# Optimization experiments

Hardware: AMD Instinct MI355X
Metric: run time of the kernel (lower is better)

The kernel has to match this reference:

```python
import jax, jax.numpy as jnp
import numpy as np

B, H, L, E, MODES = 32, 8, 4096, 64, 64


def setup_inputs() -> dict:
    key = jax.random.key(0)
    kx, kw, ki = jax.random.split(key, 3)
    x = jax.random.normal(kx, (B, H, L, E), dtype=jnp.float32)
    # nn.Parameter(torch.randn(E, E, modes, 2) / sqrt(E))
    weights = jax.random.normal(kw, (E, E, MODES, 2), dtype=jnp.float32) / np.sqrt(E)
    # register_buffer: sorted random permutation of [0, seq_len//2) truncated to modes (unique)
    index = jnp.sort(jax.random.permutation(ki, L // 2)[:MODES]).astype(jnp.int64)
    return {"x": x, "weights": weights, "index": index}


def reference(x, weights, index):
    # x: [B, H, L, E]
    Bs, Hs, Ls, Es = x.shape
    xt = jnp.swapaxes(x, -1, -2)                 # [B, H, E, L]
    x_ft = jnp.fft.rfft(xt, axis=-1)             # [B, H, E, L//2+1] complex64
    w_c = weights[..., 0] + 1j * weights[..., 1]  # [E, E, modes] complex
    sel = x_ft[..., index]                       # gather selected modes: [B, H, E, modes]
    out_sel = jnp.einsum('bhei,eoi->bhoi', sel, w_c)  # [B, H, E_out, modes]
    out_ft = jnp.zeros_like(x_ft).at[..., index].set(out_sel)  # scatter into zero spectrum
    y = jnp.fft.irfft(out_ft, n=Ls, axis=-1)     # [B, H, E, L]
    return jnp.swapaxes(y, -1, -2)               # [B, H, L, E]
```

## Files before the change

### kernel.cpp

```cpp
#include <hip/hip_runtime.h>
#include <hip/hip_bf16.h>
#include <math.h>

#define LTOT   4096
#define EDIM   64
#define NMODES 64
#define BH     256
#define TWO_PI 6.28318530717958647692f

typedef float f32x4 __attribute__((ext_vector_type(4)));
typedef short s16x8 __attribute__((ext_vector_type(8)));

__device__ inline unsigned short f2bf(float f) {
    unsigned u = __builtin_bit_cast(unsigned, f);
    u += 0x7fff + ((u >> 16) & 1);
    return (unsigned short)(u >> 16);
}
__device__ inline unsigned packbf(float lo, float hi) {
    float2 t; t.x = lo; t.y = hi;
    __hip_bfloat162 h = __float22bfloat162_rn(t);
    unsigned r;
    __builtin_memcpy(&r, &h, 4);
    return r;
}
__device__ inline float bf2f(unsigned lo16) {
    return __builtin_bit_cast(float, lo16 << 16);
}

__global__ void k_tab_m(const int* __restrict__ index, unsigned short* __restrict__ Tm) {
    int k = blockIdx.x;
    int f = index[k];
    for (int l = threadIdx.x; l < LTOT; l += blockDim.x) {
        int m = (f * l) & (LTOT - 1);
        float th = (float)m * (TWO_PI / (float)LTOT);
        float s, c; sincosf(th, &s, &c);
        Tm[(size_t)(2 * k) * LTOT + l]     = f2bf(c);
        Tm[(size_t)(2 * k + 1) * LTOT + l] = f2bf(-s);
    }
}
__global__ void k_tab_t(const int* __restrict__ index, unsigned short* __restrict__ Tt) {
    int l = blockIdx.x * 4 + (threadIdx.x >> 6);
    int k = threadIdx.x & 63;
    int f = index[k];
    int m = (f * l) & (LTOT - 1);
    float th = (float)m * (TWO_PI / (float)LTOT);
    float s, c; sincosf(th, &s, &c);
    ((unsigned*)Tt)[l * 64 + k] = packbf(c, s);
}
__global__ void k_wtab(const float* __restrict__ w, unsigned* __restrict__ wt) {
    int i = blockIdx.x * 256 + threadIdx.x;
    float2 v = ((const float2*)w)[i];
    wt[i] = packbf(v.x, v.y);
}

__global__ __launch_bounds__(256, 4) void k_stage1(const float* __restrict__ x,
                                                   const unsigned short* __restrict__ Tm,
                                                   float* __restrict__ Xp) {
    int bh = blockIdx.x >> 2, part = blockIdx.x & 3;
    const float* xb = x + ((size_t)bh * LTOT + part * 1024) * EDIM;
    __shared__ unsigned xT[2][64 * 68];

    int t = threadIdx.x;
    int q = t & 15, lp0 = t >> 4;
    int lane = t & 63, w = t >> 6;
    int r = lane & 15, kb8 = lane >> 4;
    int es = w & 1, ms = w >> 1;
    unsigned swzW = ((unsigned)(q & 7)) << 2;

    f32x4 acc[2][4];
    #pragma unroll
    for (int i = 0; i < 2; ++i)
        #pragma unroll
        for (int n = 0; n < 4; ++n) acc[i][n] = (f32x4)0.f;

    float4 xn[8];
    #pragma unroll
    for (int p = 0; p < 4; ++p) {
        const float* b = xb + (size_t)(2 * (lp0 + p * 16)) * EDIM + 4 * q;
        xn[2 * p]     = *(const float4*)b;
        xn[2 * p + 1] = *(const float4*)(b + EDIM);
    }
    #pragma unroll
    for (int p = 0; p < 4; ++p) {
        float A0[4] = {xn[2*p].x, xn[2*p].y, xn[2*p].z, xn[2*p].w};
        float A1[4] = {xn[2*p+1].x, xn[2*p+1].y, xn[2*p+1].z, xn[2*p+1].w};
        #pragma unroll
        for (int j = 0; j < 4; ++j)
            xT[0][(4 * q + j) * 68 + (((unsigned)(lp0 + p * 16)) ^ swzW)] = packbf(A0[j], A1[j]);
    }
    __syncthreads();

    for (int t8 = 0; t8 < 8; ++t8) {
        int cur = t8 & 1;
        if (t8 < 7) {
            const float* tb = xb + (size_t)((t8 + 1) * 128) * EDIM;
            #pragma unroll
            for (int p = 0; p < 4; ++p) {
                const float* b = tb + (size_t)(2 * (lp0 + p * 16)) * EDIM + 4 * q;
                xn[2 * p]     = *(const float4*)b;
                xn[2 * p + 1] = *(const float4*)(b + EDIM);
            }
        }
        #pragma unroll
        for (int kk = 0; kk < 4; ++kk) {
            s16x8 af[2];
            #pragma unroll
            for (int sub = 0; sub < 2; ++sub) {
                int row = es * 32 + sub * 16 + r;
                unsigned swz = (((unsigned)sub) << 4) + (((unsigned)(r >> 2)) << 2);
                af[sub] = *(const s16x8*)(xT[cur] + row * 68 + (((unsigned)(kk * 16 + kb8 * 4)) ^ swz));
            }
            #pragma unroll
            for (int ns = 0; ns < 4; ++ns) {
                int m = ms * 64 + ns * 16 + r;
                s16x8 bf = *(const s16x8*)(Tm + (size_t)m * LTOT + part * 1024 + t8 * 128 + kk * 32 + kb8 * 8);
                acc[0][ns] = __builtin_amdgcn_mfma_f32_16x16x32_bf16(af[0], bf, acc[0][ns], 0, 0, 0);
                acc[1][ns] = __builtin_amdgcn_mfma_f32_16x16x32_bf16(af[1], bf, acc[1][ns], 0, 0, 0);
            }
        }
        if (t8 < 7) {
            #pragma unroll
            for (int p = 0; p < 4; ++p) {
                float A0[4] = {xn[2*p].x, xn[2*p].y, xn[2*p].z, xn[2*p].w};
                float A1[4] = {xn[2*p+1].x, xn[2*p+1].y, xn[2*p+1].z, xn[2*p+1].w};
                #pragma unroll
                for (int j = 0; j < 4; ++j)
                    xT[cur ^ 1][(4 * q + j) * 68 + (((unsigned)(lp0 + p * 16)) ^ swzW)] = packbf(A0[j], A1[j]);
            }
        }
        __syncthreads();
    }

    float* Xb = Xp + ((size_t)part * BH + bh) * (64 * 128);
    #pragma unroll
    for (int sub = 0; sub < 2; ++sub)
        #pragma unroll
        for (int ns = 0; ns < 4; ++ns)
            #pragma unroll
            for (int g = 0; g < 4; ++g)
                Xb[(es * 32 + sub * 16 + kb8 * 4 + g) * 128 + ms * 64 + ns * 16 + r] = acc[sub][ns][g];
}

__global__ __launch_bounds__(512, 4) void k_stage23(const float* __restrict__ Xp,
                                                    const unsigned* __restrict__ wtab,
                                                    const unsigned short* __restrict__ Tt,
                                                    const int* __restrict__ index,
                                                    float* __restrict__ y) {
    int bh = blockIdx.x;
    __shared__ float XsR[64 * 68];
    __shared__ float XsI[64 * 68];
    __shared__ unsigned ABl[64 * 68];

    int t = threadIdx.x;
    int lane = t & 63, w = t >> 6;
    int r = lane & 15, kb8 = lane >> 4;

    #pragma unroll
    for (int i = 0; i < 4; ++i) {
        int idx = t + i * 512;
        f32x4 v = (f32x4)0.f;
        #pragma unroll
        for (int p = 0; p < 4; ++p)
            v += ((const f32x4*)(Xp + ((size_t)p * BH + bh) * 8192))[idx];
        int e = idx >> 5, k0 = (idx & 31) * 2;
        XsR[e * 68 + k0]     = v.x;
        XsI[e * 68 + k0]     = v.y;
        XsR[e * 68 + k0 + 1] = v.z;
        XsI[e * 68 + k0 + 1] = v.w;
    }
    __syncthreads();

    {
        int k = lane;
        int f = index[k];
        float cc = (f == 0 ? 1.0f : 2.0f) / (float)LTOT;
        int o0 = w * 8;
        float aR[8] = {}, aI[8] = {};
        for (int e = 0; e < 64; ++e) {
            float xr = XsR[e * 68 + k];
            float xi = XsI[e * 68 + k];
            #pragma unroll
            for (int oi = 0; oi < 8; ++oi) {
                unsigned wv = wtab[((size_t)(e * 64 + o0 + oi)) * 64 + k];
                float wr = bf2f(wv & 0xffffu);
                float wi = bf2f(wv >> 16);
                aR[oi] += xr * wr - xi * wi;
                aI[oi] += xr * wi + xi * wr;
            }
        }
        #pragma unroll
        for (int oi = 0; oi < 8; ++oi) {
            float im = (f == 0) ? 0.0f : -cc * aI[oi];
            ABl[(o0 + oi) * 68 + k] = packbf(cc * aR[oi], im);
        }
    }
    __syncthreads();

    s16x8 afr[4][4];
    #pragma unroll
    for (int es2 = 0; es2 < 4; ++es2)
        #pragma unroll
        for (int ks = 0; ks < 4; ++ks)
            afr[es2][ks] = *(const s16x8*)((const unsigned short*)ABl +
                                           (es2 * 16 + r) * 136 + ks * 32 + kb8 * 8);

    for (int it = 0; it < 32; ++it) {
        int ltile = w * 512 + it * 16;
        s16x8 btf[4];
        #pragma unroll
        for (int ks = 0; ks < 4; ++ks)
            btf[ks] = *(const s16x8*)(Tt + (size_t)(ltile + r) * 128 + ks * 32 + kb8 * 8);
        f32x4 oa[4];
        #pragma unroll
        for (int es2 = 0; es2 < 4; ++es2) oa[es2] = (f32x4)0.f;
        #pragma unroll
        for (int ks = 0; ks < 4; ++ks)
            #pragma unroll
            for (int es2 = 0; es2 < 4; ++es2)
                oa[es2] = __builtin_amdgcn_mfma_f32_16x16x32_bf16(afr[es2][ks], btf[ks], oa[es2], 0, 0, 0);
        float* yb = y + ((size_t)bh * LTOT + ltile + r) * EDIM;
        #pragma unroll
        for (int es2 = 0; es2 < 4; ++es2)
            *(f32x4*)(yb + es2 * 16 + kb8 * 4) = oa[es2];
    }
}

extern "C" void kernel_launch(void* const* d_in, const int* in_sizes, int n_in,
                              void* d_out, int out_size, void* d_ws, size_t ws_size,
                              hipStream_t stream) {
    const float* x     = (const float*)d_in[0];
    const float* wgt   = (const float*)d_in[1];
    const int*   index = (const int*)d_in[2];
    float* y  = (float*)d_out;
    float* ws = (float*)d_ws;

    unsigned short* Tm = (unsigned short*)ws;
    unsigned short* Tt = (unsigned short*)(ws + 262144);
    unsigned*       wt = (unsigned*)(ws + 524288);
    float*          Xp = ws + 786432;

    hipLaunchKernelGGL(k_tab_m,   dim3(NMODES), dim3(256), 0, stream, index, Tm);
    hipLaunchKernelGGL(k_tab_t,   dim3(1024),   dim3(256), 0, stream, index, Tt);
    hipLaunchKernelGGL(k_wtab,    dim3(1024),   dim3(256), 0, stream, wgt, wt);
    hipLaunchKernelGGL(k_stage1,  dim3(BH * 4), dim3(256), 0, stream, x, Tm, Xp);
    hipLaunchKernelGGL(k_stage23, dim3(BH),     dim3(512), 0, stream, Xp, wt, Tt, index, y);
}
```

Measured before the change: 220.7 us.

## Merge table kernels, single-buffer stage1 LDS, split stage23 into more-parallel stage2/stage3

The three table-building kernels become one launch. Stage1 drops its double-buffered LDS tile for a single buffer with an extra barrier, and raises the occupancy hint to 5 blocks. The fused stage23 kernel, which ran only 256 blocks, is split into a mixing kernel that writes bf16 coefficients to global memory and a synthesis kernel with 4x as many blocks, to use more CUs for the output-bound inverse transform. The cost is an extra launch, a global round trip for the coefficients, and less overlap of loads with compute in stage1.

```diff
diff --git a/kernel.cpp b/kernel.cpp
--- a/kernel.cpp
+++ b/kernel.cpp
@@ -27,38 +27,41 @@
     return __builtin_bit_cast(float, lo16 << 16);
 }
 
-__global__ void k_tab_m(const int* __restrict__ index, unsigned short* __restrict__ Tm) {
-    int k = blockIdx.x;
-    int f = index[k];
-    for (int l = threadIdx.x; l < LTOT; l += blockDim.x) {
+__global__ __launch_bounds__(256) void k_tables(const int* __restrict__ index,
+                                                const float* __restrict__ w,
+                                                unsigned short* __restrict__ Tm,
+                                                unsigned short* __restrict__ Tt,
+                                                unsigned* __restrict__ wt) {
+    int b = blockIdx.x, t = threadIdx.x;
+    if (b < 64) {
+        int k = b, f = index[k];
+        for (int l = t; l < LTOT; l += 256) {
+            int m = (f * l) & (LTOT - 1);
+            float th = (float)m * (TWO_PI / (float)LTOT);
+            float s, c; sincosf(th, &s, &c);
+            Tm[(size_t)(2 * k) * LTOT + l]     = f2bf(c);
+            Tm[(size_t)(2 * k + 1) * LTOT + l] = f2bf(-s);
+        }
+    } else if (b < 64 + 1024) {
+        int l = (b - 64) * 4 + (t >> 6);
+        int k = t & 63, f = index[k];
         int m = (f * l) & (LTOT - 1);
         float th = (float)m * (TWO_PI / (float)LTOT);
         float s, c; sincosf(th, &s, &c);
-        Tm[(size_t)(2 * k) * LTOT + l]     = f2bf(c);
-        Tm[(size_t)(2 * k + 1) * LTOT + l] = f2bf(-s);
-    }
-}
-__global__ void k_tab_t(const int* __restrict__ index, unsigned short* __restrict__ Tt) {
-    int l = blockIdx.x * 4 + (threadIdx.x >> 6);
-    int k = threadIdx.x & 63;
-    int f = index[k];
-    int m = (f * l) & (LTOT - 1);
-    float th = (float)m * (TWO_PI / (float)LTOT);
-    float s, c; sincosf(th, &s, &c);
-    ((unsigned*)Tt)[l * 64 + k] = packbf(c, s);
-}
-__global__ void k_wtab(const float* __restrict__ w, unsigned* __restrict__ wt) {
-    int i = blockIdx.x * 256 + threadIdx.x;
-    float2 v = ((const float2*)w)[i];
-    wt[i] = packbf(v.x, v.y);
-}
-
-__global__ __launch_bounds__(256, 4) void k_stage1(const float* __restrict__ x,
+        ((unsigned*)Tt)[l * 64 + k] = packbf(c, s);
+    } else {
+        int i = (b - 1088) * 256 + t;
+        float2 v = ((const float2*)w)[i];
+        wt[i] = packbf(v.x, v.y);
+    }
+}
+
+__global__ __launch_bounds__(256, 5) void k_stage1(const float* __restrict__ x,
                                                    const unsigned short* __restrict__ Tm,
                                                    float* __restrict__ Xp) {
     int bh = blockIdx.x >> 2, part = blockIdx.x & 3;
     const float* xb = x + ((size_t)bh * LTOT + part * 1024) * EDIM;
-    __shared__ unsigned xT[2][64 * 68];
+    __shared__ unsigned xT[64 * 68];
 
     int t = threadIdx.x;
     int q = t & 15, lp0 = t >> 4;
@@ -74,31 +77,31 @@
         for (int n = 0; n < 4; ++n) acc[i][n] = (f32x4)0.f;
 
     float4 xn[8];
-    #pragma unroll
-    for (int p = 0; p < 4; ++p) {
-        const float* b = xb + (size_t)(2 * (lp0 + p * 16)) * EDIM + 4 * q;
-        xn[2 * p]     = *(const float4*)b;
-        xn[2 * p + 1] = *(const float4*)(b + EDIM);
-    }
-    #pragma unroll
-    for (int p = 0; p < 4; ++p) {
-        float A0[4] = {xn[2*p].x, xn[2*p].y, xn[2*p].z, xn[2*p].w};
-        float A1[4] = {xn[2*p+1].x, xn[2*p+1].y, xn[2*p+1].z, xn[2*p+1].w};
-        #pragma unroll
-        for (int j = 0; j < 4; ++j)
-            xT[0][(4 * q + j) * 68 + (((unsigned)(lp0 + p * 16)) ^ swzW)] = packbf(A0[j], A1[j]);
-    }
-    __syncthreads();
-
+    {
+        #pragma unroll
+        for (int p = 0; p < 4; ++p) {
+            const float* bp = xb + (size_t)(2 * (lp0 + p * 16)) * EDIM + 4 * q;
+            xn[2 * p]     = *(const float4*)bp;
+            xn[2 * p + 1] = *(const float4*)(bp + EDIM);
+        }
+    }
     for (int t8 = 0; t8 < 8; ++t8) {
-        int cur = t8 & 1;
+        #pragma unroll
+        for (int p = 0; p < 4; ++p) {
+            float A0[4] = {xn[2*p].x, xn[2*p].y, xn[2*p].z, xn[2*p].w};
+            float A1[4] = {xn[2*p+1].x, xn[2*p+1].y, xn[2*p+1].z, xn[2*p+1].w};
+            #pragma unroll
+            for (int j = 0; j < 4; ++j)
+                xT[(4 * q + j) * 68 + (((unsigned)(lp0 + p * 16)) ^ swzW)] = packbf(A0[j], A1[j]);
+        }
+        __syncthreads();
         if (t8 < 7) {
             const float* tb = xb + (size_t)((t8 + 1) * 128) * EDIM;
             #pragma unroll
             for (int p = 0; p < 4; ++p) {
-                const float* b = tb + (size_t)(2 * (lp0 + p * 16)) * EDIM + 4 * q;
-                xn[2 * p]     = *(const float4*)b;
-                xn[2 * p + 1] = *(const float4*)(b + EDIM);
+                const float* bp = tb + (size_t)(2 * (lp0 + p * 16)) * EDIM + 4 * q;
+                xn[2 * p]     = *(const float4*)bp;
+                xn[2 * p + 1] = *(const float4*)(bp + EDIM);
             }
         }
         #pragma unroll
@@ -108,7 +111,7 @@
             for (int sub = 0; sub < 2; ++sub) {
                 int row = es * 32 + sub * 16 + r;
                 unsigned swz = (((unsigned)sub) << 4) + (((unsigned)(r >> 2)) << 2);
-                af[sub] = *(const s16x8*)(xT[cur] + row * 68 + (((unsigned)(kk * 16 + kb8 * 4)) ^ swz));
+                af[sub] = *(const s16x8*)(xT + row * 68 + (((unsigned)(kk * 16 + kb8 * 4)) ^ swz));
             }
             #pragma unroll
             for (int ns = 0; ns < 4; ++ns) {
@@ -118,16 +121,6 @@
                 acc[1][ns] = __builtin_amdgcn_mfma_f32_16x16x32_bf16(af[1], bf, acc[1][ns], 0, 0, 0);
             }
         }
-        if (t8 < 7) {
-            #pragma unroll
-            for (int p = 0; p < 4; ++p) {
-                float A0[4] = {xn[2*p].x, xn[2*p].y, xn[2*p].z, xn[2*p].w};
-                float A1[4] = {xn[2*p+1].x, xn[2*p+1].y, xn[2*p+1].z, xn[2*p+1].w};
-                #pragma unroll
-                for (int j = 0; j < 4; ++j)
-                    xT[cur ^ 1][(4 * q + j) * 68 + (((unsigned)(lp0 + p * 16)) ^ swzW)] = packbf(A0[j], A1[j]);
-            }
-        }
         __syncthreads();
     }
 
@@ -141,19 +134,14 @@
                 Xb[(es * 32 + sub * 16 + kb8 * 4 + g) * 128 + ms * 64 + ns * 16 + r] = acc[sub][ns][g];
 }
 
-__global__ __launch_bounds__(512, 4) void k_stage23(const float* __restrict__ Xp,
-                                                    const unsigned* __restrict__ wtab,
-                                                    const unsigned short* __restrict__ Tt,
-                                                    const int* __restrict__ index,
-                                                    float* __restrict__ y) {
+__global__ __launch_bounds__(512) void k_stage2(const float* __restrict__ Xp,
+                                                const unsigned* __restrict__ wtab,
+                                                const int* __restrict__ index,
+                                                unsigned* __restrict__ ABo) {
     int bh = blockIdx.x;
     __shared__ float XsR[64 * 68];
     __shared__ float XsI[64 * 68];
-    __shared__ unsigned ABl[64 * 68];
-
     int t = threadIdx.x;
-    int lane = t & 63, w = t >> 6;
-    int r = lane & 15, kb8 = lane >> 4;
 
     #pragma unroll
     for (int i = 0; i < 4; ++i) {
@@ -170,58 +158,77 @@
     }
     __syncthreads();
 
+    int k = t & 63, og = t >> 6;
+    int f = index[k];
+    float cc = (f == 0 ? 1.0f : 2.0f) / (float)LTOT;
+    int o0 = og * 8;
+    float aR[8] = {}, aI[8] = {};
+    for (int e = 0; e < 64; ++e) {
+        float xr = XsR[e * 68 + k];
+        float xi = XsI[e * 68 + k];
+        #pragma unroll
+        for (int oi = 0; oi < 8; ++oi) {
+            unsigned wv = wtab[((size_t)(e * 64 + o0 + oi)) * 64 + k];
+            float wr = bf2f(wv & 0xffffu);
+            float wi = bf2f(wv >> 16);
+            aR[oi] += xr * wr - xi * wi;
+            aI[oi] += xr * wi + xi * wr;
+        }
+    }
+    #pragma unroll
+    for (int oi = 0; oi < 8; ++oi) {
+        float im = (f == 0) ? 0.0f : -cc * aI[oi];
+        ABo[((size_t)bh * 64 + o0 + oi) * 64 + k] = packbf(cc * aR[oi], im);
+    }
+}
+
+#define S3P16 136
+__global__ __launch_bounds__(256, 4) void k_stage3(const unsigned short* __restrict__ Tt,
+                                                   const unsigned* __restrict__ ABo,
+                                                   float* __restrict__ y) {
+    int bh = blockIdx.x >> 2, qtr = blockIdx.x & 3;
+    __shared__ unsigned short ABl[64 * S3P16];
+    int t = threadIdx.x;
+    int lane = t & 63, wave = t >> 6;
+    int r = lane & 15, kb8 = lane >> 4;
+
     {
-        int k = lane;
-        int f = index[k];
-        float cc = (f == 0 ? 1.0f : 2.0f) / (float)LTOT;
-        int o0 = w * 8;
-        float aR[8] = {}, aI[8] = {};
-        for (int e = 0; e < 64; ++e) {
-            float xr = XsR[e * 68 + k];
-            float xi = XsI[e * 68 + k];
-            #pragma unroll
-            for (int oi = 0; oi < 8; ++oi) {
-                unsigned wv = wtab[((size_t)(e * 64 + o0 + oi)) * 64 + k];
-                float wr = bf2f(wv & 0xffffu);
-                float wi = bf2f(wv >> 16);
-                aR[oi] += xr * wr - xi * wi;
-                aI[oi] += xr * wi + xi * wr;
-            }
-        }
-        #pragma unroll
-        for (int oi = 0; oi < 8; ++oi) {
-            float im = (f == 0) ? 0.0f : -cc * aI[oi];
-            ABl[(o0 + oi) * 68 + k] = packbf(cc * aR[oi], im);
+        const unsigned* src = ABo + (size_t)bh * 4096;
+        unsigned* dst = (unsigned*)ABl;
+        #pragma unroll
+        for (int i = 0; i < 16; ++i) {
+            int idx = t + i * 256;
+            int o = idx >> 6, c = idx & 63;
+            dst[o * (S3P16 / 2) + c] = src[idx];
         }
     }
     __syncthreads();
 
     s16x8 afr[4][4];
     #pragma unroll
-    for (int es2 = 0; es2 < 4; ++es2)
+    for (int es = 0; es < 4; ++es)
         #pragma unroll
         for (int ks = 0; ks < 4; ++ks)
-            afr[es2][ks] = *(const s16x8*)((const unsigned short*)ABl +
-                                           (es2 * 16 + r) * 136 + ks * 32 + kb8 * 8);
-
-    for (int it = 0; it < 32; ++it) {
-        int ltile = w * 512 + it * 16;
+            afr[es][ks] = *(const s16x8*)(ABl + (es * 16 + r) * S3P16 + ks * 32 + kb8 * 8);
+
+    for (int it = 0; it < 16; ++it) {
+        int ltile = qtr * 1024 + it * 64 + wave * 16;
         s16x8 btf[4];
         #pragma unroll
         for (int ks = 0; ks < 4; ++ks)
             btf[ks] = *(const s16x8*)(Tt + (size_t)(ltile + r) * 128 + ks * 32 + kb8 * 8);
-        f32x4 oa[4];
-        #pragma unroll
-        for (int es2 = 0; es2 < 4; ++es2) oa[es2] = (f32x4)0.f;
+        f32x4 acc[4];
+        #pragma unroll
+        for (int es = 0; es < 4; ++es) acc[es] = (f32x4)0.f;
         #pragma unroll
         for (int ks = 0; ks < 4; ++ks)
             #pragma unroll
-            for (int es2 = 0; es2 < 4; ++es2)
-                oa[es2] = __builtin_amdgcn_mfma_f32_16x16x32_bf16(afr[es2][ks], btf[ks], oa[es2], 0, 0, 0);
+            for (int es = 0; es < 4; ++es)
+                acc[es] = __builtin_amdgcn_mfma_f32_16x16x32_bf16(afr[es][ks], btf[ks], acc[es], 0, 0, 0);
         float* yb = y + ((size_t)bh * LTOT + ltile + r) * EDIM;
         #pragma unroll
-        for (int es2 = 0; es2 < 4; ++es2)
-            *(f32x4*)(yb + es2 * 16 + kb8 * 4) = oa[es2];
+        for (int es = 0; es < 4; ++es)
+            *(f32x4*)(yb + es * 16 + kb8 * 4) = acc[es];
     }
 }
 
@@ -238,10 +245,10 @@
     unsigned short* Tt = (unsigned short*)(ws + 262144);
     unsigned*       wt = (unsigned*)(ws + 524288);
     float*          Xp = ws + 786432;
-
-    hipLaunchKernelGGL(k_tab_m,   dim3(NMODES), dim3(256), 0, stream, index, Tm);
-    hipLaunchKernelGGL(k_tab_t,   dim3(1024),   dim3(256), 0, stream, index, Tt);
-    hipLaunchKernelGGL(k_wtab,    dim3(1024),   dim3(256), 0, stream, wgt, wt);
-    hipLaunchKernelGGL(k_stage1,  dim3(BH * 4), dim3(256), 0, stream, x, Tm, Xp);
-    hipLaunchKernelGGL(k_stage23, dim3(BH),     dim3(512), 0, stream, Xp, wt, Tt, index, y);
-}
+    unsigned*       ABo = (unsigned*)(ws + 9175040);
+
+    hipLaunchKernelGGL(k_tables, dim3(2112),   dim3(256), 0, stream, index, wgt, Tm, Tt, wt);
+    hipLaunchKernelGGL(k_stage1, dim3(BH * 4), dim3(256), 0, stream, x, Tm, Xp);
+    hipLaunchKernelGGL(k_stage2, dim3(BH),     dim3(512), 0, stream, Xp, wt, index, ABo);
+    hipLaunchKernelGGL(k_stage3, dim3(BH * 4), dim3(256), 0, stream, Tt, ABo, y);
+}
```

After: 226.2 us. 1.03x slower.
